# Kernel tuning notes

Hardware: AMD Instinct MI355X
Metric: run time of the kernel (lower is better)

Reference implementation:

```python
import jax, jax.numpy as jnp
import numpy as np

B, S, D, H, DFF = 2, 2048, 768, 12, 3072
DK = D // H
LN_EPS = 1e-5

def _row_norm(x):
    # L2-normalize along last dim (torch F.normalize semantics)
    n = jnp.sqrt(jnp.sum(x * x, axis=-1, keepdims=True))
    return x / jnp.maximum(n, 1e-12)

def _layer_norm(x, gamma, beta):
    mu = jnp.mean(x, axis=-1, keepdims=True)
    var = jnp.mean((x - mu) ** 2, axis=-1, keepdims=True)
    return (x - mu) * jax.lax.rsqrt(var + LN_EPS) * gamma + beta

def setup_inputs() -> dict:
    key = jax.random.key(0)
    ks = jax.random.split(key, 16)
    sd = 1.0 / np.sqrt(D)
    sf = 1.0 / np.sqrt(DFF)
    inp = {
        "x": jax.random.normal(ks[0], (B, S, D), jnp.float32),
        "Wq": jax.random.uniform(ks[1], (D, D), jnp.float32, -sd, sd),
        "bq": jnp.zeros((D,), jnp.float32),
        "Wk": jax.random.uniform(ks[2], (D, D), jnp.float32, -sd, sd),
        "bk": jnp.zeros((D,), jnp.float32),
        "Wv": jax.random.uniform(ks[3], (D, D), jnp.float32, -sd, sd),
        "bv": jnp.zeros((D,), jnp.float32),
        "Wo": jax.random.uniform(ks[4], (D, D), jnp.float32, -sd, sd),
        "bo": jnp.zeros((D,), jnp.float32),
        "W1": jax.random.uniform(ks[5], (D, DFF), jnp.float32, -sd, sd),
        "b1": jnp.zeros((DFF,), jnp.float32),
        "W2": jax.random.uniform(ks[6], (DFF, D), jnp.float32, -sf, sf),
        "b2": jnp.zeros((D,), jnp.float32),
        "gamma": jnp.ones((D,), jnp.float32),
        "beta": jnp.zeros((D,), jnp.float32),
    }
    return inp

def reference(x, Wq, bq, Wk, bk, Wv, bv, Wo, bo, W1, b1, W2, b2, gamma, beta):
    b, s = x.shape[0], x.shape[1]
    # QKV projections, split into heads: [B,H,S,DK]
    def heads(y):
        return y.reshape(b, s, H, DK).transpose(0, 2, 1, 3)
    Q = heads(x @ Wq + bq)
    K = heads(x @ Wk + bk)
    V = heads(x @ Wv + bv)
    Qn = _row_norm(Q)
    Kn = _row_norm(K)
    scores = jnp.einsum("bhqd,bhkd->bhqk", Qn, Kn)
    attn = scores * scores  # squared dot-product, no softmax
    out = jnp.einsum("bhqk,bhkd->bhqd", attn, V)
    out = out.transpose(0, 2, 1, 3).reshape(b, s, D)
    attn_out = out @ Wo + bo
    x = _layer_norm(x + attn_out, gamma, beta)
    # FFN with exact GELU
    h = jax.nn.gelu(x @ W1 + b1, approximate=False)
    ff = h @ W2 + b2
    x = _layer_norm(x + ff, gamma, beta)  # norm1 reused
    return x
```

## Files before the change

kernel.cpp:

```cpp
#include <hip/hip_runtime.h>
#include <math.h>


using bf16   = __bf16;
using bf16x8 = __attribute__((ext_vector_type(8))) __bf16;
using bf16x4 = __attribute__((ext_vector_type(4))) __bf16;
using f32x4  = __attribute__((ext_vector_type(4))) float;

constexpr int S_   = 2048;
constexpr int D_   = 768;
constexpr int DFF_ = 3072;
constexpr int M_   = 4096;
constexpr int BH_  = 24;

__device__ __forceinline__ f32x4 mfma16(bf16x8 a, bf16x8 b, f32x4 c) {
    return __builtin_amdgcn_mfma_f32_16x16x32_bf16(a, b, c, 0, 0, 0);
}

__device__ __forceinline__ void gload16(const bf16* g, bf16* l) {
    __builtin_amdgcn_global_load_lds(
        (const __attribute__((address_space(1))) void*)g,
        (__attribute__((address_space(3))) void*)l, 16, 0, 0);
}

template<int N> __device__ __forceinline__ void wait_vmcnt() {
    if constexpr (N == 0)      asm volatile("s_waitcnt vmcnt(0)" ::: "memory");
    else if constexpr (N == 4) asm volatile("s_waitcnt vmcnt(4)" ::: "memory");
    else if constexpr (N == 8) asm volatile("s_waitcnt vmcnt(8)" ::: "memory");
    else static_assert(N == 0, "unsupported vmcnt");
}
__device__ __forceinline__ void wait_lgkm0() {
    asm volatile("s_waitcnt lgkmcnt(0)" ::: "memory");
}

__device__ __forceinline__ int xcd_swz(int orig, int nwg) {
    return (orig & 7) * (nwg >> 3) + (orig >> 3);
}

__device__ __forceinline__ float gelu_f(float v) {
    float y = 1.5957691f * (v + 0.044715f * v * v * v);
    return v / (1.0f + __expf(-y));
}

__global__ __launch_bounds__(256)
void pack_x_kernel(const float* __restrict__ x, bf16* __restrict__ xb) {
    const int i = blockIdx.x * 256 + threadIdx.x;
    float4 v = ((const float4*)x)[i];
    bf16x4 o;
    o[0] = (bf16)v.x; o[1] = (bf16)v.y; o[2] = (bf16)v.z; o[3] = (bf16)v.w;
    ((bf16x4*)xb)[i] = o;
}

__global__ __launch_bounds__(256)
void wt_all_kernel(const float* __restrict__ Wq, const float* __restrict__ Wk,
                   const float* __restrict__ Wv, const float* __restrict__ Wo,
                   const float* __restrict__ W1, const float* __restrict__ W2,
                   bf16* __restrict__ Wqkvt, bf16* __restrict__ Wot,
                   bf16* __restrict__ W1t, bf16* __restrict__ W2t) {
    int bid = blockIdx.x;
    const float* in; bf16* out; int K, N, t;
    if (bid < 576) {
        int m = bid / 144; t = bid % 144; K = 768; N = 768;
        in  = (m == 0) ? Wq : (m == 1) ? Wk : (m == 2) ? Wv : Wo;
        out = (m == 3) ? Wot : Wqkvt + (size_t)m * 768 * 768;
    } else if (bid < 1152) {
        t = bid - 576; K = 768; N = 3072; in = W1; out = W1t;
    } else {
        t = bid - 1152; K = 3072; N = 768; in = W2; out = W2t;
    }
    const int ntx = N / 64;
    const int n0 = (t % ntx) * 64, k0 = (t / ntx) * 64;

    __shared__ __align__(16) bf16 T[64][72];
    const int tt = threadIdx.x;
    const int r  = tt >> 2, c0 = (tt & 3) * 16;
    const float* src = in + (size_t)(k0 + r) * N + n0 + c0;
#pragma unroll
    for (int j = 0; j < 16; j += 4) {
        float4 v = *(const float4*)(src + j);
        T[r][c0 + j + 0] = (bf16)v.x;
        T[r][c0 + j + 1] = (bf16)v.y;
        T[r][c0 + j + 2] = (bf16)v.z;
        T[r][c0 + j + 3] = (bf16)v.w;
    }
    __syncthreads();
    bf16x8 o0, o1;
#pragma unroll
    for (int j = 0; j < 8; j++) { o0[j] = T[c0 + j][r]; o1[j] = T[c0 + 8 + j][r]; }
    bf16* dst = out + (size_t)(n0 + r) * K + k0 + c0;
    *(bf16x8*)(dst)     = o0;
    *(bf16x8*)(dst + 8) = o1;
}

template<int EPI, int K, int BM, int BN, int WR, int WC>
__global__ __launch_bounds__(256)
void gemm_bt(const bf16* __restrict__ A, const bf16* __restrict__ Bt,
             const float* __restrict__ bias0, const float* __restrict__ bias1,
             const float* __restrict__ bias2, const float* __restrict__ residf,
             const bf16* __restrict__ residb, bf16* __restrict__ outb,
             bf16* __restrict__ qo, bf16* __restrict__ ko, bf16* __restrict__ vo) {
    constexpr int MR  = BM / WR / 16;
    constexpr int NR  = BN / WC / 16;
    constexpr int GA  = BM / 32;
    constexpr int GB  = BN / 32;
    constexpr int NPT = GA + GB;
    constexpr int NCOL = (EPI == 0) ? 2304 : (EPI == 2) ? 3072 : 768;
    constexpr int NBX  = NCOL / BN;
    __shared__ __align__(16) bf16 Al[2 * BM * 64];
    __shared__ __align__(16) bf16 Bl[2 * BN * 64];
    const int tid  = threadIdx.x;
    const int lane = tid & 63, w = tid >> 6;
    const int wr = w / WC, wc = w % WC;
    const int wg = xcd_swz(blockIdx.x, gridDim.x);
    const int m0 = (wg / NBX) * BM, n0 = (wg % NBX) * BN;
    const int g = lane >> 4, q = lane & 15;
    const int srow = lane >> 3;
    const int schunk = (((lane & 7) ^ ((lane >> 3) & 7))) * 8;

    f32x4 acc[MR][NR] = {};

    const bf16* gaA = A  + (long)(m0 + w * (BM / 4) + srow) * K + schunk;
    const bf16* gaB = Bt + (long)(n0 + w * (BN / 4) + srow) * K + schunk;

    auto stage = [&](int buf, int kt) {
#pragma unroll
        for (int i = 0; i < GA; i++)
            gload16(gaA + kt + (long)i * 8 * K,
                    &Al[buf * BM * 64 + (w * (BM / 4) + i * 8) * 64]);
#pragma unroll
        for (int i = 0; i < GB; i++)
            gload16(gaB + kt + (long)i * 8 * K,
                    &Bl[buf * BN * 64 + (w * (BN / 4) + i * 8) * 64]);
    };
    auto compute = [&](int buf) {
#pragma unroll
        for (int c = 0; c < 2; c++) {
            const int rch = ((c * 4 + g) ^ (q & 7)) * 8;
            bf16x8 af[MR], bfr[NR];
#pragma unroll
            for (int i = 0; i < MR; i++)
                af[i] = *(const bf16x8*)
                    &Al[buf * BM * 64 + (wr * (BM / WR) + i * 16 + q) * 64 + rch];
#pragma unroll
            for (int i = 0; i < NR; i++)
                bfr[i] = *(const bf16x8*)
                    &Bl[buf * BN * 64 + (wc * (BN / WC) + i * 16 + q) * 64 + rch];
#pragma unroll
            for (int mi = 0; mi < MR; mi++)
#pragma unroll
                for (int ni = 0; ni < NR; ni++)
                    acc[mi][ni] = mfma16(af[mi], bfr[ni], acc[mi][ni]);
        }
    };

    stage(0, 0);
    stage(1, 64);
    int cur = 0;
    for (int kt = 0; kt < K - 64; kt += 64) {
        wait_vmcnt<NPT>();
        __builtin_amdgcn_s_barrier();
        compute(cur);
        wait_lgkm0();
        __builtin_amdgcn_s_barrier();
        if (kt + 128 < K) stage(cur, kt + 128);
        cur ^= 1;
    }
    wait_vmcnt<0>();
    __builtin_amdgcn_s_barrier();
    compute(cur);

#pragma unroll
    for (int mi = 0; mi < MR; mi++) {
        if (EPI == 0) {
            const int col0  = n0 + wc * 64;
            const int which = (col0 >= 1536) ? 2 : (col0 >= 768 ? 1 : 0);
            const int row0  = m0 + wr * (BM / WR) + mi * 16 + g * 4;
            float val[NR][4];
#pragma unroll
            for (int ni = 0; ni < NR; ni++) {
                const int dd = col0 + ni * 16 + q - which * 768;
                const float bias = (which == 0 ? bias0 : which == 1 ? bias1 : bias2)[dd];
#pragma unroll
                for (int r = 0; r < 4; r++) val[ni][r] = acc[mi][ni][r] + bias;
            }
            if (which <= 1) {
#pragma unroll
                for (int r = 0; r < 4; r++) {
                    float ss = val[0][r] * val[0][r];
#pragma unroll
                    for (int ni = 1; ni < NR; ni++) ss += val[ni][r] * val[ni][r];
                    ss += __shfl_xor(ss, 1);
                    ss += __shfl_xor(ss, 2);
                    ss += __shfl_xor(ss, 4);
                    ss += __shfl_xor(ss, 8);
                    const float rn = 1.0f / fmaxf(sqrtf(ss), 1e-12f);
#pragma unroll
                    for (int ni = 0; ni < NR; ni++) val[ni][r] *= rn;
                }
            }
            const int dd0 = col0 - which * 768;
            const int hh  = dd0 >> 6;
            const long bh = (long)(row0 >> 11) * 12 + hh;
#pragma unroll
            for (int ni = 0; ni < NR; ni++) {
                const int dk = ni * 16 + q;
                if (which == 2) {
                    bf16x4 pv;
#pragma unroll
                    for (int r = 0; r < 4; r++) pv[r] = (bf16)val[ni][r];
                    *(bf16x4*)&vo[(bh * 64 + dk) * 2048 + (row0 & 2047)] = pv;
                } else {
                    bf16* dst = (which == 0) ? qo : ko;
#pragma unroll
                    for (int r = 0; r < 4; r++)
                        dst[(bh * 2048 + ((row0 + r) & 2047)) * 64 + dk] = (bf16)val[ni][r];
                }
            }
        } else {
#pragma unroll
            for (int ni = 0; ni < NR; ni++) {
                const int col  = n0 + wc * (BN / WC) + ni * 16 + q;
                const int row0 = m0 + wr * (BM / WR) + mi * 16 + g * 4;
                const float bias = bias0[col];
                if (EPI == 1) {
#pragma unroll
                    for (int r = 0; r < 4; r++) {
                        const int row = row0 + r;
                        outb[(long)row * 768 + col] =
                            (bf16)(acc[mi][ni][r] + bias + residf[(long)row * 768 + col]);
                    }
                } else if (EPI == 3) {
#pragma unroll
                    for (int r = 0; r < 4; r++) {
                        const int row = row0 + r;
                        outb[(long)row * 768 + col] =
                            (bf16)(acc[mi][ni][r] + bias + (float)residb[(long)row * 768 + col]);
                    }
                } else {
#pragma unroll
                    for (int r = 0; r < 4; r++) {
                        const float v = acc[mi][ni][r] + bias;
                        outb[(long)(row0 + r) * 3072 + col] = (bf16)gelu_f(v);
                    }
                }
            }
        }
    }
}

__global__ __launch_bounds__(256, 2)
void attn_kernel(const bf16* __restrict__ Qn, const bf16* __restrict__ Kn,
                 const bf16* __restrict__ Vt, bf16* __restrict__ AO) {
    const int wg  = xcd_swz(blockIdx.x, gridDim.x);
    const int bh  = wg >> 4;
    const int tid = threadIdx.x, lane = tid & 63, w = tid >> 6;
    const int g = lane >> 4, q15 = lane & 15;
    const int qbase = (wg & 15) * 128 + w * 32;

    __shared__ __align__(16) bf16 Kl[2][64][72];
    __shared__ __align__(16) bf16 Vl[2][64][72];
    __shared__ __align__(16) bf16 Pl[4][32][72];
    bf16 (*Pw)[72] = Pl[w];

    const bf16* Qp = Qn + (long)bh * S_ * 64;
    const bf16* Kp = Kn + (long)bh * S_ * 64;
    const bf16* Vp = Vt + (long)bh * 64 * S_;

    const int srow = tid >> 3, scol = (tid & 7) * 8;

    bf16x8 qf00 = *(const bf16x8*)&Qp[(long)(qbase + q15) * 64 + g * 8];
    bf16x8 qf01 = *(const bf16x8*)&Qp[(long)(qbase + q15) * 64 + 32 + g * 8];
    bf16x8 qf10 = *(const bf16x8*)&Qp[(long)(qbase + 16 + q15) * 64 + g * 8];
    bf16x8 qf11 = *(const bf16x8*)&Qp[(long)(qbase + 16 + q15) * 64 + 32 + g * 8];

    f32x4 o0[4] = {}, o1[4] = {};

    bf16x8 aK0, aK1, aV0, aV1, bK0, bK1, bV0, bV1;
    auto gloadA = [&](int kt) {
        aK0 = *(const bf16x8*)&Kp[(long)(kt + srow) * 64 + scol];
        aK1 = *(const bf16x8*)&Kp[(long)(kt + 32 + srow) * 64 + scol];
        aV0 = *(const bf16x8*)&Vp[(long)srow * S_ + kt + scol];
        aV1 = *(const bf16x8*)&Vp[(long)(32 + srow) * S_ + kt + scol];
    };
    auto gloadB = [&](int kt) {
        bK0 = *(const bf16x8*)&Kp[(long)(kt + srow) * 64 + scol];
        bK1 = *(const bf16x8*)&Kp[(long)(kt + 32 + srow) * 64 + scol];
        bV0 = *(const bf16x8*)&Vp[(long)srow * S_ + kt + scol];
        bV1 = *(const bf16x8*)&Vp[(long)(32 + srow) * S_ + kt + scol];
    };
    auto stageA = [&](int buf) {
        *(bf16x8*)&Kl[buf][srow][scol]      = aK0;
        *(bf16x8*)&Kl[buf][32 + srow][scol] = aK1;
        *(bf16x8*)&Vl[buf][srow][scol]      = aV0;
        *(bf16x8*)&Vl[buf][32 + srow][scol] = aV1;
    };
    auto stageB = [&](int buf) {
        *(bf16x8*)&Kl[buf][srow][scol]      = bK0;
        *(bf16x8*)&Kl[buf][32 + srow][scol] = bK1;
        *(bf16x8*)&Vl[buf][srow][scol]      = bV0;
        *(bf16x8*)&Vl[buf][32 + srow][scol] = bV1;
    };

    auto compute = [&](int cur) {
        bf16x8 kf[4][2];
#pragma unroll
        for (int ni = 0; ni < 4; ni++)
#pragma unroll
            for (int c = 0; c < 2; c++)
                kf[ni][c] = *(const bf16x8*)&Kl[cur][ni * 16 + q15][c * 32 + g * 8];
        f32x4 s0[4], s1[4];
#pragma unroll
        for (int ni = 0; ni < 4; ni++) {
            s0[ni] = mfma16(kf[ni][0], qf00, f32x4{0.f, 0.f, 0.f, 0.f});
            s0[ni] = mfma16(kf[ni][1], qf01, s0[ni]);
            s1[ni] = mfma16(kf[ni][0], qf10, f32x4{0.f, 0.f, 0.f, 0.f});
            s1[ni] = mfma16(kf[ni][1], qf11, s1[ni]);
        }
#pragma unroll
        for (int ni = 0; ni < 4; ni++) {
            bf16x4 p0, p1;
#pragma unroll
            for (int r = 0; r < 4; r++) {
                float v0 = s0[ni][r]; p0[r] = (bf16)(v0 * v0);
                float v1 = s1[ni][r]; p1[r] = (bf16)(v1 * v1);
            }
            *(bf16x4*)&Pw[q15][ni * 16 + g * 4]      = p0;
            *(bf16x4*)&Pw[16 + q15][ni * 16 + g * 4] = p1;
        }
        bf16x8 pf00 = *(const bf16x8*)&Pw[q15][g * 8];
        bf16x8 pf01 = *(const bf16x8*)&Pw[q15][32 + g * 8];
        bf16x8 pf10 = *(const bf16x8*)&Pw[16 + q15][g * 8];
        bf16x8 pf11 = *(const bf16x8*)&Pw[16 + q15][32 + g * 8];
        bf16x8 vf[4][2];
#pragma unroll
        for (int ni = 0; ni < 4; ni++)
#pragma unroll
            for (int c = 0; c < 2; c++)
                vf[ni][c] = *(const bf16x8*)&Vl[cur][ni * 16 + q15][c * 32 + g * 8];
#pragma unroll
        for (int ni = 0; ni < 4; ni++) {
            o0[ni] = mfma16(pf00, vf[ni][0], o0[ni]);
            o0[ni] = mfma16(pf01, vf[ni][1], o0[ni]);
            o1[ni] = mfma16(pf10, vf[ni][0], o1[ni]);
            o1[ni] = mfma16(pf11, vf[ni][1], o1[ni]);
        }
    };

    gloadA(0);
    stageA(0);
    gloadB(64);
    __syncthreads();
    for (int t = 0; t <= 28; t += 2) {
        stageB(1);
        gloadA((t + 2) * 64);
        compute(0);
        __syncthreads();
        stageA(0);
        if (t + 3 < 32) gloadB((t + 3) * 64);
        compute(1);
        __syncthreads();
    }
    stageB(1);
    compute(0);
    __syncthreads();
    compute(1);

    const int b = bh / 12, h = bh % 12;
#pragma unroll
    for (int ni = 0; ni < 4; ni++)
#pragma unroll
        for (int r = 0; r < 4; r++) {
            const int s0r = qbase + g * 4 + r;
            AO[((long)b * S_ + s0r) * D_ + h * 64 + ni * 16 + q15] = (bf16)o0[ni][r];
            const int s1r = qbase + 16 + g * 4 + r;
            AO[((long)b * S_ + s1r) * D_ + h * 64 + ni * 16 + q15] = (bf16)o1[ni][r];
        }
}

template<bool WB>
__global__ __launch_bounds__(256)
void ln_kernel(const bf16* __restrict__ y, const float* __restrict__ gamma,
               const float* __restrict__ beta, float* __restrict__ xo,
               bf16* __restrict__ xob) {
    __shared__ float sa[4], sb[4];
    const int row = blockIdx.x, t = threadIdx.x;
    const bf16* yr = y + (long)row * 768;
    float v0 = (float)yr[t], v1 = (float)yr[t + 256], v2 = (float)yr[t + 512];
    float s  = v0 + v1 + v2;
    float ss = v0 * v0 + v1 * v1 + v2 * v2;
#pragma unroll
    for (int o = 32; o; o >>= 1) { s += __shfl_xor(s, o); ss += __shfl_xor(ss, o); }
    if ((t & 63) == 0) { sa[t >> 6] = s; sb[t >> 6] = ss; }
    __syncthreads();
    s  = sa[0] + sa[1] + sa[2] + sa[3];
    ss = sb[0] + sb[1] + sb[2] + sb[3];
    const float mu   = s * (1.0f / 768.0f);
    const float var  = ss * (1.0f / 768.0f) - mu * mu;
    const float rstd = rsqrtf(var + 1e-5f);
#pragma unroll
    for (int i = 0; i < 3; i++) {
        const int c = t + i * 256;
        const float vv = (i == 0) ? v0 : (i == 1) ? v1 : v2;
        const float ov = (vv - mu) * rstd * gamma[c] + beta[c];
        if (WB) xob[(long)row * 768 + c] = (bf16)ov;
        else    xo[(long)row * 768 + c] = ov;
    }
}

extern "C" void kernel_launch(void* const* d_in, const int* in_sizes, int n_in,
                              void* d_out, int out_size, void* d_ws, size_t ws_size,
                              hipStream_t stream) {
    const float* x     = (const float*)d_in[0];
    const float* Wq    = (const float*)d_in[1];
    const float* bq    = (const float*)d_in[2];
    const float* Wk    = (const float*)d_in[3];
    const float* bk    = (const float*)d_in[4];
    const float* Wv    = (const float*)d_in[5];
    const float* bv    = (const float*)d_in[6];
    const float* Wo    = (const float*)d_in[7];
    const float* bo    = (const float*)d_in[8];
    const float* W1    = (const float*)d_in[9];
    const float* b1    = (const float*)d_in[10];
    const float* W2    = (const float*)d_in[11];
    const float* b2    = (const float*)d_in[12];
    const float* gamma = (const float*)d_in[13];
    const float* beta  = (const float*)d_in[14];

    char* p = (char*)d_ws;
    auto alloc = [&](size_t bytes) -> void* {
        void* r = p;
        p += (bytes + 255) & ~(size_t)255;
        return r;
    };
    bf16*  Xb    = (bf16*)alloc((size_t)M_ * D_ * 2);
    bf16*  Wqkvt = (bf16*)alloc((size_t)2304 * 768 * 2);
    bf16*  Wot   = (bf16*)alloc((size_t)768 * 768 * 2);
    bf16*  W1t   = (bf16*)alloc((size_t)3072 * 768 * 2);
    bf16*  W2t   = (bf16*)alloc((size_t)768 * 3072 * 2);
    bf16*  Qh    = (bf16*)alloc((size_t)BH_ * S_ * 64 * 2);
    bf16*  Kh    = (bf16*)alloc((size_t)BH_ * S_ * 64 * 2);
    bf16*  Vt    = (bf16*)alloc((size_t)BH_ * S_ * 64 * 2);
    bf16*  AO    = (bf16*)alloc((size_t)M_ * D_ * 2);
    bf16*  y1b   = (bf16*)alloc((size_t)M_ * D_ * 2);
    bf16*  x1b   = (bf16*)alloc((size_t)M_ * D_ * 2);
    bf16*  hbuf  = (bf16*)alloc((size_t)M_ * DFF_ * 2);
    bf16*  y2b   = y1b;

    pack_x_kernel<<<(M_ * D_) / 1024, 256, 0, stream>>>(x, Xb);
    wt_all_kernel<<<1728, 256, 0, stream>>>(Wq, Wk, Wv, Wo, W1, W2,
                                            Wqkvt, Wot, W1t, W2t);

    gemm_bt<0, 768, 128, 128, 2, 2><<<18 * 32, 256, 0, stream>>>(
        Xb, Wqkvt, bq, bk, bv, nullptr, nullptr, nullptr, Qh, Kh, Vt);

    attn_kernel<<<16 * BH_, 256, 0, stream>>>(Qh, Kh, Vt, AO);

    gemm_bt<1, 768, 64, 64, 2, 2><<<12 * 64, 256, 0, stream>>>(
        AO, Wot, bo, nullptr, nullptr, x, nullptr, y1b, nullptr, nullptr, nullptr);
    ln_kernel<true><<<M_, 256, 0, stream>>>(y1b, gamma, beta, nullptr, x1b);

    gemm_bt<2, 768, 128, 128, 2, 2><<<24 * 32, 256, 0, stream>>>(
        x1b, W1t, b1, nullptr, nullptr, nullptr, nullptr, hbuf, nullptr, nullptr, nullptr);
    gemm_bt<3, 3072, 64, 64, 2, 2><<<12 * 64, 256, 0, stream>>>(
        hbuf, W2t, b2, nullptr, nullptr, nullptr, x1b, y2b, nullptr, nullptr, nullptr);
    ln_kernel<false><<<M_, 256, 0, stream>>>(y2b, gamma, beta, (float*)d_out, nullptr);
}
```

Before: 180.9 us.

## Split attention KV range across two workgroups and merge partial outputs

Doubles the attention grid by giving each workgroup half of the key/value sequence and writing two partial bf16 outputs, which a new merge kernel then sums. The goal is better occupancy and load balance, since the old grid of 384 workgroups underfilled the GPU. The P scratch buffer is halved by reusing it for both 16-row query halves, and launch bounds are raised to 3 waves per SIMD. The cost is an extra kernel launch, extra partial-output memory traffic, and one more bf16 rounding of the partial sums before they are added.

```diff
diff --git a/kernel.cpp b/kernel.cpp
--- a/kernel.cpp
+++ b/kernel.cpp
@@ -1,6 +1,5 @@
 #include <hip/hip_runtime.h>
 #include <math.h>
-
 
 using bf16   = __bf16;
 using bf16x8 = __attribute__((ext_vector_type(8))) __bf16;
@@ -49,6 +48,18 @@
     bf16x4 o;
     o[0] = (bf16)v.x; o[1] = (bf16)v.y; o[2] = (bf16)v.z; o[3] = (bf16)v.w;
     ((bf16x4*)xb)[i] = o;
+}
+
+__global__ __launch_bounds__(256)
+void merge_ao_kernel(const bf16* __restrict__ a, const bf16* __restrict__ b,
+                     bf16* __restrict__ o) {
+    const long i = ((long)blockIdx.x * 256 + threadIdx.x) * 8;
+    bf16x8 va = *(const bf16x8*)&a[i];
+    bf16x8 vb = *(const bf16x8*)&b[i];
+    bf16x8 vo;
+#pragma unroll
+    for (int j = 0; j < 8; j++) vo[j] = (bf16)((float)va[j] + (float)vb[j]);
+    *(bf16x8*)&o[i] = vo;
 }
 
 __global__ __launch_bounds__(256)
@@ -248,23 +259,29 @@
     }
 }
 
-__global__ __launch_bounds__(256, 2)
+__global__ __launch_bounds__(256, 3)
 void attn_kernel(const bf16* __restrict__ Qn, const bf16* __restrict__ Kn,
-                 const bf16* __restrict__ Vt, bf16* __restrict__ AO) {
+                 const bf16* __restrict__ Vt, bf16* __restrict__ AOp) {
     const int wg  = xcd_swz(blockIdx.x, gridDim.x);
-    const int bh  = wg >> 4;
+    const int bh  = wg >> 5;
+    const int rem = wg & 31;
+    const int kvhalf = rem >> 4;
+    const int qblk   = rem & 15;
     const int tid = threadIdx.x, lane = tid & 63, w = tid >> 6;
     const int g = lane >> 4, q15 = lane & 15;
-    const int qbase = (wg & 15) * 128 + w * 32;
+    const int qbase = qblk * 128 + w * 32;
+    const int kv0   = kvhalf * 1024;
+    constexpr int NT = 16;
 
     __shared__ __align__(16) bf16 Kl[2][64][72];
     __shared__ __align__(16) bf16 Vl[2][64][72];
-    __shared__ __align__(16) bf16 Pl[4][32][72];
+    __shared__ __align__(16) bf16 Pl[4][16][72];
     bf16 (*Pw)[72] = Pl[w];
 
     const bf16* Qp = Qn + (long)bh * S_ * 64;
-    const bf16* Kp = Kn + (long)bh * S_ * 64;
-    const bf16* Vp = Vt + (long)bh * 64 * S_;
+    const bf16* Kp = Kn + (long)bh * S_ * 64 + (long)kv0 * 64;
+    const bf16* Vp = Vt + (long)bh * 64 * S_ + kv0;
+    bf16* AOo = AOp + (long)kvhalf * M_ * D_;
 
     const int srow = tid >> 3, scol = (tid & 7) * 8;
 
@@ -318,19 +335,22 @@
         }
 #pragma unroll
         for (int ni = 0; ni < 4; ni++) {
-            bf16x4 p0, p1;
-#pragma unroll
-            for (int r = 0; r < 4; r++) {
-                float v0 = s0[ni][r]; p0[r] = (bf16)(v0 * v0);
-                float v1 = s1[ni][r]; p1[r] = (bf16)(v1 * v1);
-            }
-            *(bf16x4*)&Pw[q15][ni * 16 + g * 4]      = p0;
-            *(bf16x4*)&Pw[16 + q15][ni * 16 + g * 4] = p1;
+            bf16x4 p0;
+#pragma unroll
+            for (int r = 0; r < 4; r++) { float v = s0[ni][r]; p0[r] = (bf16)(v * v); }
+            *(bf16x4*)&Pw[q15][ni * 16 + g * 4] = p0;
         }
         bf16x8 pf00 = *(const bf16x8*)&Pw[q15][g * 8];
         bf16x8 pf01 = *(const bf16x8*)&Pw[q15][32 + g * 8];
-        bf16x8 pf10 = *(const bf16x8*)&Pw[16 + q15][g * 8];
-        bf16x8 pf11 = *(const bf16x8*)&Pw[16 + q15][32 + g * 8];
+#pragma unroll
+        for (int ni = 0; ni < 4; ni++) {
+            bf16x4 p1;
+#pragma unroll
+            for (int r = 0; r < 4; r++) { float v = s1[ni][r]; p1[r] = (bf16)(v * v); }
+            *(bf16x4*)&Pw[q15][ni * 16 + g * 4] = p1;
+        }
+        bf16x8 pf10 = *(const bf16x8*)&Pw[q15][g * 8];
+        bf16x8 pf11 = *(const bf16x8*)&Pw[q15][32 + g * 8];
         bf16x8 vf[4][2];
 #pragma unroll
         for (int ni = 0; ni < 4; ni++)
@@ -350,13 +370,13 @@
     stageA(0);
     gloadB(64);
     __syncthreads();
-    for (int t = 0; t <= 28; t += 2) {
+    for (int t = 0; t <= NT - 4; t += 2) {
         stageB(1);
         gloadA((t + 2) * 64);
         compute(0);
         __syncthreads();
         stageA(0);
-        if (t + 3 < 32) gloadB((t + 3) * 64);
+        if (t + 3 < NT) gloadB((t + 3) * 64);
         compute(1);
         __syncthreads();
     }
@@ -371,9 +391,9 @@
 #pragma unroll
         for (int r = 0; r < 4; r++) {
             const int s0r = qbase + g * 4 + r;
-            AO[((long)b * S_ + s0r) * D_ + h * 64 + ni * 16 + q15] = (bf16)o0[ni][r];
+            AOo[((long)b * S_ + s0r) * D_ + h * 64 + ni * 16 + q15] = (bf16)o0[ni][r];
             const int s1r = qbase + 16 + g * 4 + r;
-            AO[((long)b * S_ + s1r) * D_ + h * 64 + ni * 16 + q15] = (bf16)o1[ni][r];
+            AOo[((long)b * S_ + s1r) * D_ + h * 64 + ni * 16 + q15] = (bf16)o1[ni][r];
         }
 }
 
@@ -440,6 +460,7 @@
     bf16*  Qh    = (bf16*)alloc((size_t)BH_ * S_ * 64 * 2);
     bf16*  Kh    = (bf16*)alloc((size_t)BH_ * S_ * 64 * 2);
     bf16*  Vt    = (bf16*)alloc((size_t)BH_ * S_ * 64 * 2);
+    bf16*  AOp   = (bf16*)alloc((size_t)2 * M_ * D_ * 2);
     bf16*  AO    = (bf16*)alloc((size_t)M_ * D_ * 2);
     bf16*  y1b   = (bf16*)alloc((size_t)M_ * D_ * 2);
     bf16*  x1b   = (bf16*)alloc((size_t)M_ * D_ * 2);
@@ -453,7 +474,9 @@
     gemm_bt<0, 768, 128, 128, 2, 2><<<18 * 32, 256, 0, stream>>>(
         Xb, Wqkvt, bq, bk, bv, nullptr, nullptr, nullptr, Qh, Kh, Vt);
 
-    attn_kernel<<<16 * BH_, 256, 0, stream>>>(Qh, Kh, Vt, AO);
+    attn_kernel<<<2 * 16 * BH_, 256, 0, stream>>>(Qh, Kh, Vt, AOp);
+    merge_ao_kernel<<<(M_ * D_) / 2048, 256, 0, stream>>>(
+        AOp, AOp + (size_t)M_ * D_, AO);
 
     gemm_bt<1, 768, 64, 64, 2, 2><<<12 * 64, 256, 0, stream>>>(
         AO, Wot, bo, nullptr, nullptr, x, nullptr, y1b, nullptr, nullptr, nullptr);
```

Measured after the change: 175.1 us. -3.2%, faster.
